# Kernel tuning notes

Measured on AMD Instinct MI355X. Metric: run time of the kernel, lower is better.

## Reference

```python
import jax, jax.numpy as jnp
import numpy as np

DEPTH = 6
IN_FEATURES = 256
NUM_TREES = 256
TREE_DIM = 1
BATCH = 2048


def sparsemax(X, axis=0):
    """Full-sort sparsemax projection along `axis` (k=None path of the torch code)."""
    X = jnp.moveaxis(X, axis, -1)
    Xs = X - jnp.max(X, axis=-1, keepdims=True)
    z = -jnp.sort(-Xs, axis=-1)                      # descending sort
    cs = jnp.cumsum(z, axis=-1) - 1.0                # topk_cumsum - 1
    d = X.shape[-1]
    rho = jnp.arange(1, d + 1, dtype=X.dtype)
    support = rho * z > cs
    k = jnp.sum(support, axis=-1, keepdims=True)     # support size (int)
    tau = jnp.take_along_axis(cs, k - 1, axis=-1) / k.astype(X.dtype)
    out = jnp.maximum(Xs - tau, 0.0)
    return jnp.moveaxis(out, -1, axis)


def sparsemoid(x):
    return jnp.clip(0.5 * x + 0.5, 0.0, 1.0)


def bin_codes_1hot(depth, dtype=jnp.float32):
    idx = jnp.arange(2 ** depth)
    off = 2 ** jnp.arange(depth)
    codes = ((idx[None, :] // off[:, None]) % 2).astype(dtype)   # [depth, 2^depth]
    return jnp.stack([codes, 1.0 - codes], axis=-1)              # [depth, 2^depth, 2]


def setup_inputs() -> dict:
    key = jax.random.key(0)
    k1, k2, k3, k4, k5 = jax.random.split(key, 5)
    x = jax.random.normal(k1, (BATCH, IN_FEATURES), dtype=jnp.float32)
    response = jax.random.normal(k2, (NUM_TREES, TREE_DIM, 2 ** DEPTH), dtype=jnp.float32)
    feature_selection_logits = jax.random.uniform(k3, (IN_FEATURES, NUM_TREES, DEPTH), dtype=jnp.float32)
    feature_thresholds = 0.5 * jax.random.normal(k4, (NUM_TREES, DEPTH), dtype=jnp.float32)
    log_temperatures = jnp.zeros((NUM_TREES, DEPTH), dtype=jnp.float32)
    return {
        "x": x,
        "response": response,
        "feature_selection_logits": feature_selection_logits,
        "feature_thresholds": feature_thresholds,
        "log_temperatures": log_temperatures,
    }


def reference(x, response, feature_selection_logits, feature_thresholds, log_temperatures):
    depth = feature_thresholds.shape[-1]
    codes = bin_codes_1hot(depth, x.dtype)                          # [d, 2^d, 2]
    # sparsemax feature routing over the feature axis
    fs = sparsemax(feature_selection_logits, axis=0)                # [F, T, d]
    fv = jnp.einsum('bi,ind->bnd', x, fs)                           # [B, T, d]
    tl = (fv - feature_thresholds) * jnp.exp(-log_temperatures)     # [B, T, d]
    bins = sparsemoid(jnp.stack([-tl, tl], axis=-1))                # [B, T, d, 2]
    bin_matches = jnp.einsum('btds,dcs->btdc', bins, codes)         # [B, T, d, 2^d]
    response_weights = jnp.prod(bin_matches, axis=-2)               # [B, T, 2^d]
    out = jnp.einsum('bnd,ncd->bnc', response_weights, response)    # [B, T, C]
    return out.reshape(out.shape[0], -1)                            # flatten_output=True
```

## Files before the change

kernel.cpp:

```cpp
#include <hip/hip_runtime.h>
#include <math.h>

#define NF 256
#define NT 256
#define ND 6
#define NB 2048
#define NCOL (NT * ND)
#define NLEAF 64

typedef __attribute__((ext_vector_type(8))) short bf16x8;
typedef __attribute__((ext_vector_type(4))) float f32x4;
typedef __attribute__((ext_vector_type(8))) unsigned short u16x8;

__device__ inline unsigned short f2bf(float f) {
    unsigned u = __float_as_uint(f);
    u += 0x7fffu + ((u >> 16) & 1u);
    return (unsigned short)(u >> 16);
}
__device__ inline float bf2f(unsigned short h) {
    return __uint_as_float(((unsigned)h) << 16);
}

__global__ __launch_bounds__(256) void sparsemax_michelot(
    const float* __restrict__ fsl,
    unsigned short* __restrict__ fs_hi,
    unsigned short* __restrict__ fs_lo)
{
    const int lane = threadIdx.x & 63;
    const int col  = blockIdx.x * 4 + (threadIdx.x >> 6);

    float x[4];
    #pragma unroll
    for (int j = 0; j < 4; j++)
        x[j] = fsl[(lane + 64 * j) * NCOL + col];

    float mx = fmaxf(fmaxf(x[0], x[1]), fmaxf(x[2], x[3]));
    #pragma unroll
    for (int off = 32; off > 0; off >>= 1)
        mx = fmaxf(mx, __shfl_xor(mx, off));
    #pragma unroll
    for (int j = 0; j < 4; j++) x[j] -= mx;

    float s = (x[0] + x[1]) + (x[2] + x[3]);
    #pragma unroll
    for (int off = 32; off > 0; off >>= 1)
        s += __shfl_xor(s, off);
    float tau = (s - 1.0f) / 256.0f;

    int prev = 256;
    for (int it = 0; it < 64; it++) {
        float ss = 0.0f, cc = 0.0f;
        #pragma unroll
        for (int j = 0; j < 4; j++)
            if (x[j] > tau) { ss += x[j]; cc += 1.0f; }
        #pragma unroll
        for (int off = 32; off > 0; off >>= 1) {
            ss += __shfl_xor(ss, off);
            cc += __shfl_xor(cc, off);
        }
        const int c = (int)cc;
        if (c == prev) break;
        prev = c;
        tau = (ss - 1.0f) / cc;
    }

    #pragma unroll
    for (int j = 0; j < 4; j++) {
        const float v = fmaxf(x[j] - tau, 0.0f);
        const unsigned short h = f2bf(v);
        fs_hi[col * NF + lane + 64 * j] = h;
        fs_lo[col * NF + lane + 64 * j] = f2bf(v - bf2f(h));
    }
}

#define TM 64
#define TN 96
#define TK 32
#define PK (TK + 8)

union SMem {
    struct {
        unsigned short Ah[TM][PK], Al[TM][PK];
        unsigned short Bh[TN][PK], Bl[TN][PK];
    } st;
    struct {
        float fv[TM][TN + 1];
        float resp[16][NLEAF];
    } ep;
};

__global__ __launch_bounds__(256) void gemm_tree_kernel(
    const float* __restrict__ x,
    const unsigned short* __restrict__ Bh,
    const unsigned short* __restrict__ Bl,
    const float* __restrict__ thr,
    const float* __restrict__ ltemp,
    const float* __restrict__ resp_g,
    float* __restrict__ out)
{
    __shared__ SMem sm;

    const int tid  = threadIdx.x;
    const int lane = tid & 63;
    const int w    = tid >> 6;
    const int wm   = w & 1;
    const int wn   = w >> 1;
    const int bm0  = blockIdx.y * TM;
    const int bn0  = blockIdx.x * TN;
    const int t0   = blockIdx.x * 16;

    const int l15  = lane & 15;
    const int quad = lane >> 4;

    const int arow  = tid >> 2;
    const int akseg = (tid & 3) * 8;
    const int bhalf = tid >> 7;
    const int brow  = (tid & 127) >> 2;
    const int bkseg = (tid & 3) * 8;

    f32x4 acc[2][3] = {};

    for (int k0 = 0; k0 < NF; k0 += TK) {
        {
            const float4 v0 = *(const float4*)&x[(bm0 + arow) * NF + k0 + akseg];
            const float4 v1 = *(const float4*)&x[(bm0 + arow) * NF + k0 + akseg + 4];
            const float vv[8] = {v0.x, v0.y, v0.z, v0.w, v1.x, v1.y, v1.z, v1.w};
            u16x8 hi, lo;
            #pragma unroll
            for (int j = 0; j < 8; j++) {
                const unsigned short h = f2bf(vv[j]);
                hi[j] = h;
                lo[j] = f2bf(vv[j] - bf2f(h));
            }
            *(u16x8*)&sm.st.Ah[arow][akseg] = hi;
            *(u16x8*)&sm.st.Al[arow][akseg] = lo;
        }
        {
            const unsigned short* __restrict__ src = bhalf ? Bl : Bh;
            unsigned short (*dst)[PK] = bhalf ? sm.st.Bl : sm.st.Bh;
            #pragma unroll
            for (int c = 0; c < 3; c++) {
                const int row = c * 32 + brow;
                *(u16x8*)&dst[row][bkseg] =
                    *(const u16x8*)&src[(bn0 + row) * NF + k0 + bkseg];
            }
        }
        __syncthreads();

        #pragma unroll
        for (int im = 0; im < 2; im++) {
            const bf16x8 a_h = *(const bf16x8*)&sm.st.Ah[wm * 32 + im * 16 + l15][quad * 8];
            const bf16x8 a_l = *(const bf16x8*)&sm.st.Al[wm * 32 + im * 16 + l15][quad * 8];
            #pragma unroll
            for (int in = 0; in < 3; in++) {
                const bf16x8 b_h = *(const bf16x8*)&sm.st.Bh[wn * 48 + in * 16 + l15][quad * 8];
                const bf16x8 b_l = *(const bf16x8*)&sm.st.Bl[wn * 48 + in * 16 + l15][quad * 8];
                acc[im][in] = __builtin_amdgcn_mfma_f32_16x16x32_bf16(a_h, b_h, acc[im][in], 0, 0, 0);
                acc[im][in] = __builtin_amdgcn_mfma_f32_16x16x32_bf16(a_h, b_l, acc[im][in], 0, 0, 0);
                acc[im][in] = __builtin_amdgcn_mfma_f32_16x16x32_bf16(a_l, b_h, acc[im][in], 0, 0, 0);
            }
        }
        __syncthreads();
    }

    #pragma unroll
    for (int im = 0; im < 2; im++)
        #pragma unroll
        for (int in = 0; in < 3; in++)
            #pragma unroll
            for (int r = 0; r < 4; r++) {
                const int m = wm * 32 + im * 16 + quad * 4 + r;
                const int n = wn * 48 + in * 16 + l15;
                sm.ep.fv[m][n] = acc[im][in][r];
            }
    {
        const int tr  = tid >> 4;
        const int seg = (tid & 15) * 4;
        *(float4*)&sm.ep.resp[tr][seg] = *(const float4*)&resp_g[(t0 + tr) * NLEAF + seg];
    }
    __syncthreads();

    #pragma unroll
    for (int i = 0; i < 4; i++) {
        const int item = tid + 256 * i;
        const int m    = item & 63;
        const int t16  = item >> 6;
        const int t    = t0 + t16;

        float sp[ND], sn[ND];
        #pragma unroll
        for (int d = 0; d < ND; d++) {
            const float f  = sm.ep.fv[m][t16 * ND + d];
            const float tl = (f - thr[t * ND + d]) * __expf(-ltemp[t * ND + d]);
            const float h  = 0.5f * tl;
            sp[d] = fminf(fmaxf(0.5f + h, 0.0f), 1.0f);
            sn[d] = fminf(fmaxf(0.5f - h, 0.0f), 1.0f);
        }

        float wleaf[NLEAF];
        wleaf[0] = 1.0f;
        #pragma unroll
        for (int d = 0; d < ND; d++) {
            const int half = 1 << d;
            #pragma unroll
            for (int c = 0; c < NLEAF / 2; c++) {
                if (c < half) {
                    const float base = wleaf[c];
                    wleaf[c + half] = base * sn[d];
                    wleaf[c]        = base * sp[d];
                }
            }
        }

        float a = 0.0f;
        #pragma unroll
        for (int c = 0; c < NLEAF; c++)
            a = fmaf(wleaf[c], sm.ep.resp[t16][c], a);

        out[(bm0 + m) * NT + t] = a;
    }
}

extern "C" void kernel_launch(void* const* d_in, const int* in_sizes, int n_in,
                              void* d_out, int out_size, void* d_ws, size_t ws_size,
                              hipStream_t stream)
{
    const float* x    = (const float*)d_in[0];
    const float* resp = (const float*)d_in[1];
    const float* fsl  = (const float*)d_in[2];
    const float* thr  = (const float*)d_in[3];
    const float* lt   = (const float*)d_in[4];
    float* out = (float*)d_out;

    unsigned short* fs_hi = (unsigned short*)d_ws;
    unsigned short* fs_lo = fs_hi + (size_t)NCOL * NF;

    sparsemax_michelot<<<NCOL / 4, 256, 0, stream>>>(fsl, fs_hi, fs_lo);

    dim3 g(NCOL / TN, NB / TM);
    gemm_tree_kernel<<<g, 256, 0, stream>>>(x, fs_hi, fs_lo, thr, lt, resp, out);
}
```

Measured before the change: 89.82 us.

## Pre-split x to bf16 hi/lo in prep kernel, hoist B frags, vectorize output stores

The fp32 to bf16 hi/lo split of x moves out of the GEMM inner loop into the prep kernel, run as extra blocks alongside the sparsemax blocks. The GEMM now loads pre-split bf16 tiles directly, so it no longer redoes the conversion once for each of the 16 column blocks. B fragments are loaded from LDS once per k-step instead of once per im iteration. Epilogue results are staged in shared memory and written as coalesced float4 rows, at the cost of extra workspace traffic and one more barrier.

```diff
diff --git a/kernel.cpp b/kernel.cpp
--- a/kernel.cpp
+++ b/kernel.cpp
@@ -21,27 +21,48 @@
     return __uint_as_float(((unsigned)h) << 16);
 }
 
-__global__ __launch_bounds__(256) void sparsemax_michelot(
+__global__ __launch_bounds__(256) void prep_kernel(
     const float* __restrict__ fsl,
+    const float* __restrict__ x,
     unsigned short* __restrict__ fs_hi,
-    unsigned short* __restrict__ fs_lo)
+    unsigned short* __restrict__ fs_lo,
+    unsigned short* __restrict__ xh,
+    unsigned short* __restrict__ xl)
 {
-    const int lane = threadIdx.x & 63;
-    const int col  = blockIdx.x * 4 + (threadIdx.x >> 6);
-
-    float x[4];
+    const int tid = threadIdx.x;
+
+    if (blockIdx.x >= 384) {
+        const int base = (blockIdx.x - 384) * 256 + tid;
+        #pragma unroll
+        for (int p = 0; p < 4; p++) {
+            const int i = (base + p * 32768) * 4;
+            const float4 v = *(const float4*)&x[i];
+            const unsigned short h0 = f2bf(v.x), h1 = f2bf(v.y),
+                                 h2 = f2bf(v.z), h3 = f2bf(v.w);
+            *(ushort4*)&xh[i] = make_ushort4(h0, h1, h2, h3);
+            *(ushort4*)&xl[i] = make_ushort4(
+                f2bf(v.x - bf2f(h0)), f2bf(v.y - bf2f(h1)),
+                f2bf(v.z - bf2f(h2)), f2bf(v.w - bf2f(h3)));
+        }
+        return;
+    }
+
+    const int lane = tid & 63;
+    const int col  = blockIdx.x * 4 + (tid >> 6);
+
+    float xv[4];
     #pragma unroll
     for (int j = 0; j < 4; j++)
-        x[j] = fsl[(lane + 64 * j) * NCOL + col];
-
-    float mx = fmaxf(fmaxf(x[0], x[1]), fmaxf(x[2], x[3]));
+        xv[j] = fsl[(lane + 64 * j) * NCOL + col];
+
+    float mx = fmaxf(fmaxf(xv[0], xv[1]), fmaxf(xv[2], xv[3]));
     #pragma unroll
     for (int off = 32; off > 0; off >>= 1)
         mx = fmaxf(mx, __shfl_xor(mx, off));
     #pragma unroll
-    for (int j = 0; j < 4; j++) x[j] -= mx;
-
-    float s = (x[0] + x[1]) + (x[2] + x[3]);
+    for (int j = 0; j < 4; j++) xv[j] -= mx;
+
+    float s = (xv[0] + xv[1]) + (xv[2] + xv[3]);
     #pragma unroll
     for (int off = 32; off > 0; off >>= 1)
         s += __shfl_xor(s, off);
@@ -52,7 +73,7 @@
         float ss = 0.0f, cc = 0.0f;
         #pragma unroll
         for (int j = 0; j < 4; j++)
-            if (x[j] > tau) { ss += x[j]; cc += 1.0f; }
+            if (xv[j] > tau) { ss += xv[j]; cc += 1.0f; }
         #pragma unroll
         for (int off = 32; off > 0; off >>= 1) {
             ss += __shfl_xor(ss, off);
@@ -66,7 +87,7 @@
 
     #pragma unroll
     for (int j = 0; j < 4; j++) {
-        const float v = fmaxf(x[j] - tau, 0.0f);
+        const float v = fmaxf(xv[j] - tau, 0.0f);
         const unsigned short h = f2bf(v);
         fs_hi[col * NF + lane + 64 * j] = h;
         fs_lo[col * NF + lane + 64 * j] = f2bf(v - bf2f(h));
@@ -86,13 +107,15 @@
     struct {
         float fv[TM][TN + 1];
         float resp[16][NLEAF];
+        float res[TM][17];
     } ep;
 };
 
 __global__ __launch_bounds__(256) void gemm_tree_kernel(
-    const float* __restrict__ x,
-    const unsigned short* __restrict__ Bh,
-    const unsigned short* __restrict__ Bl,
+    const unsigned short* __restrict__ Ahg,
+    const unsigned short* __restrict__ Alg,
+    const unsigned short* __restrict__ Bhg,
+    const unsigned short* __restrict__ Blg,
     const float* __restrict__ thr,
     const float* __restrict__ ltemp,
     const float* __restrict__ resp_g,
@@ -121,22 +144,10 @@
     f32x4 acc[2][3] = {};
 
     for (int k0 = 0; k0 < NF; k0 += TK) {
+        *(u16x8*)&sm.st.Ah[arow][akseg] = *(const u16x8*)&Ahg[(bm0 + arow) * NF + k0 + akseg];
+        *(u16x8*)&sm.st.Al[arow][akseg] = *(const u16x8*)&Alg[(bm0 + arow) * NF + k0 + akseg];
         {
-            const float4 v0 = *(const float4*)&x[(bm0 + arow) * NF + k0 + akseg];
-            const float4 v1 = *(const float4*)&x[(bm0 + arow) * NF + k0 + akseg + 4];
-            const float vv[8] = {v0.x, v0.y, v0.z, v0.w, v1.x, v1.y, v1.z, v1.w};
-            u16x8 hi, lo;
-            #pragma unroll
-            for (int j = 0; j < 8; j++) {
-                const unsigned short h = f2bf(vv[j]);
-                hi[j] = h;
-                lo[j] = f2bf(vv[j] - bf2f(h));
-            }
-            *(u16x8*)&sm.st.Ah[arow][akseg] = hi;
-            *(u16x8*)&sm.st.Al[arow][akseg] = lo;
-        }
-        {
-            const unsigned short* __restrict__ src = bhalf ? Bl : Bh;
+            const unsigned short* __restrict__ src = bhalf ? Blg : Bhg;
             unsigned short (*dst)[PK] = bhalf ? sm.st.Bl : sm.st.Bh;
             #pragma unroll
             for (int c = 0; c < 3; c++) {
@@ -147,17 +158,21 @@
         }
         __syncthreads();
 
+        bf16x8 b_h[3], b_l[3];
+        #pragma unroll
+        for (int in = 0; in < 3; in++) {
+            b_h[in] = *(const bf16x8*)&sm.st.Bh[wn * 48 + in * 16 + l15][quad * 8];
+            b_l[in] = *(const bf16x8*)&sm.st.Bl[wn * 48 + in * 16 + l15][quad * 8];
+        }
         #pragma unroll
         for (int im = 0; im < 2; im++) {
             const bf16x8 a_h = *(const bf16x8*)&sm.st.Ah[wm * 32 + im * 16 + l15][quad * 8];
             const bf16x8 a_l = *(const bf16x8*)&sm.st.Al[wm * 32 + im * 16 + l15][quad * 8];
             #pragma unroll
             for (int in = 0; in < 3; in++) {
-                const bf16x8 b_h = *(const bf16x8*)&sm.st.Bh[wn * 48 + in * 16 + l15][quad * 8];
-                const bf16x8 b_l = *(const bf16x8*)&sm.st.Bl[wn * 48 + in * 16 + l15][quad * 8];
-                acc[im][in] = __builtin_amdgcn_mfma_f32_16x16x32_bf16(a_h, b_h, acc[im][in], 0, 0, 0);
-                acc[im][in] = __builtin_amdgcn_mfma_f32_16x16x32_bf16(a_h, b_l, acc[im][in], 0, 0, 0);
-                acc[im][in] = __builtin_amdgcn_mfma_f32_16x16x32_bf16(a_l, b_h, acc[im][in], 0, 0, 0);
+                acc[im][in] = __builtin_amdgcn_mfma_f32_16x16x32_bf16(a_h, b_h[in], acc[im][in], 0, 0, 0);
+                acc[im][in] = __builtin_amdgcn_mfma_f32_16x16x32_bf16(a_h, b_l[in], acc[im][in], 0, 0, 0);
+                acc[im][in] = __builtin_amdgcn_mfma_f32_16x16x32_bf16(a_l, b_h[in], acc[im][in], 0, 0, 0);
             }
         }
         __syncthreads();
@@ -168,11 +183,9 @@
         #pragma unroll
         for (int in = 0; in < 3; in++)
             #pragma unroll
-            for (int r = 0; r < 4; r++) {
-                const int m = wm * 32 + im * 16 + quad * 4 + r;
-                const int n = wn * 48 + in * 16 + l15;
-                sm.ep.fv[m][n] = acc[im][in][r];
-            }
+            for (int r = 0; r < 4; r++)
+                sm.ep.fv[wm * 32 + im * 16 + quad * 4 + r][wn * 48 + in * 16 + l15]
+                    = acc[im][in][r];
     {
         const int tr  = tid >> 4;
         const int seg = (tid & 15) * 4;
@@ -182,10 +195,9 @@
 
     #pragma unroll
     for (int i = 0; i < 4; i++) {
-        const int item = tid + 256 * i;
-        const int m    = item & 63;
-        const int t16  = item >> 6;
-        const int t    = t0 + t16;
+        const int m   = tid & 63;
+        const int t16 = (tid >> 6) + 4 * i;
+        const int t   = t0 + t16;
 
         float sp[ND], sn[ND];
         #pragma unroll
@@ -217,7 +229,16 @@
         for (int c = 0; c < NLEAF; c++)
             a = fmaf(wleaf[c], sm.ep.resp[t16][c], a);
 
-        out[(bm0 + m) * NT + t] = a;
+        sm.ep.res[m][t16] = a;
+    }
+    __syncthreads();
+
+    {
+        const int row = tid >> 2;
+        const int j   = (tid & 3) * 4;
+        const float4 o = make_float4(sm.ep.res[row][j + 0], sm.ep.res[row][j + 1],
+                                     sm.ep.res[row][j + 2], sm.ep.res[row][j + 3]);
+        *(float4*)&out[(bm0 + row) * NT + t0 + j] = o;
     }
 }
 
@@ -234,9 +255,11 @@
 
     unsigned short* fs_hi = (unsigned short*)d_ws;
     unsigned short* fs_lo = fs_hi + (size_t)NCOL * NF;
-
-    sparsemax_michelot<<<NCOL / 4, 256, 0, stream>>>(fsl, fs_hi, fs_lo);
+    unsigned short* xh    = fs_lo + (size_t)NCOL * NF;
+    unsigned short* xl    = xh + (size_t)NB * NF;
+
+    prep_kernel<<<512, 256, 0, stream>>>(fsl, x, fs_hi, fs_lo, xh, xl);
 
     dim3 g(NCOL / TN, NB / TM);
-    gemm_tree_kernel<<<g, 256, 0, stream>>>(x, fs_hi, fs_lo, thr, lt, resp, out);
-}
+    gemm_tree_kernel<<<g, 256, 0, stream>>>(xh, xl, fs_hi, fs_lo, thr, lt, resp, out);
+}
```

After: 96.67 us. 7.6% more time.
